# Kernel optimization log

Measured on AMD Instinct MI355X. Metric: run time of the kernel, lower is better.

Reference implementation:

```python
import jax, jax.numpy as jnp
import numpy as np

N_NODES = 50000
N_EDGES = 600000
VOCAB = 50000
D_IN = 256   # embed.output_size
D = 128      # size


def gcn_conv(x, w, b, src, dst, num_nodes):
    # PyG GCNConv: x' = D^{-1/2} (A + I) D^{-1/2} (x @ W^T) + b
    loop = jnp.arange(num_nodes)
    s = jnp.concatenate([src, loop])
    d = jnp.concatenate([dst, loop])
    x = x @ w.T                                           # [N, D]
    deg = jax.ops.segment_sum(jnp.ones_like(s, x.dtype), d, num_segments=num_nodes)
    dinv = jnp.where(deg > 0, jax.lax.rsqrt(deg), 0.0)
    norm = dinv[s] * dinv[d]                              # [E+N]
    msgs = x[s] * norm[:, None]                           # gather + scale
    out = jax.ops.segment_sum(msgs, d, num_segments=num_nodes)  # scatter-add
    return out + b


def setup_inputs() -> dict:
    key = jax.random.key(0)
    ks = jax.random.split(key, 7)
    node_tokens = jax.random.randint(ks[0], (N_NODES,), 0, VOCAB)
    edge_index = jax.random.randint(ks[1], (2, N_EDGES), 0, N_NODES)
    embed_table = jax.random.normal(ks[2], (VOCAB, D_IN), dtype=jnp.float32) * 0.02
    W_node_w = jax.random.normal(ks[3], (D, D_IN), dtype=jnp.float32) * 0.02
    W_node_b = jnp.zeros((D,), dtype=jnp.float32)
    w1 = jax.random.normal(ks[4], (D, D), dtype=jnp.float32) * 0.02
    b1 = jnp.zeros((D,), dtype=jnp.float32)
    w2 = jax.random.normal(ks[5], (D, D), dtype=jnp.float32) * 0.02
    b2 = jnp.zeros((D,), dtype=jnp.float32)
    return {"node_tokens": node_tokens, "edge_index": edge_index,
            "embed_table": embed_table, "W_node_w": W_node_w, "W_node_b": W_node_b,
            "w1": w1, "b1": b1, "w2": w2, "b2": b2}


def reference(node_tokens, edge_index, embed_table, W_node_w, W_node_b, w1, b1, w2, b2):
    src, dst = edge_index[0], edge_index[1]
    e = embed_table[node_tokens]                 # [N, D_IN] embedding lookup
    x = e @ W_node_w.T + W_node_b                # [N, D]
    x = gcn_conv(x, w1, b1, src, dst, N_NODES)
    x = jax.nn.relu(x)
    x = gcn_conv(x, w2, b2, src, dst, N_NODES)
    return x
```

## Files before the change

kernel.cpp:

```cpp
#include <hip/hip_runtime.h>
#include <hip/hip_bf16.h>

#define N_NODES 50000
#define N_EDGES 600000
#define D_IN 256
#define D 128

#define SCAN_CHUNK 1024
#define N_CHUNKS ((N_NODES + SCAN_CHUNK - 1) / SCAN_CHUNK)
#define GEMM_BLOCKS ((N_NODES + 31) / 32)
#define EDGE_BLOCKS ((N_EDGES + 255) / 256)

typedef unsigned short ushort_t;
typedef __attribute__((ext_vector_type(8))) short bf16x8;
typedef __attribute__((ext_vector_type(16))) float f32x16;

__device__ __forceinline__ float bf2f(ushort_t u) {
  union { unsigned int i; float f; } v;
  v.i = ((unsigned int)u) << 16;
  return v.f;
}
__device__ __forceinline__ ushort_t f2bf(float f) {
  union { float f; unsigned int i; } v;
  v.f = f;
  unsigned int x = v.i;
  unsigned int r = (x + 0x7FFFu + ((x >> 16) & 1u)) >> 16;
  return (ushort_t)r;
}


__global__ __launch_bounds__(256) void k_prep_deg(
    const float* __restrict__ wn, const float* __restrict__ w1,
    const float* __restrict__ bn, const float* __restrict__ w2,
    const float* __restrict__ b1, const float* __restrict__ b2,
    const int* __restrict__ dst,
    ushort_t* __restrict__ WcSw, float* __restrict__ bc,
    ushort_t* __restrict__ W2Sw, float* __restrict__ b1f,
    float* __restrict__ b2f, int* __restrict__ deg,
    int* __restrict__ epos) {
  int bid = blockIdx.x;
  if (bid < 128) {
    int j = bid;
    int k = threadIdx.x;
    float acc = 0.f;
    for (int m = 0; m < 128; m++)
      acc += w1[j * 128 + m] * wn[m * 256 + k];
    ushort_t h = f2bf(acc);
    ushort_t l = f2bf(acc - bf2f(h));
    int wv = j >> 5, fm = j & 31;
    int kh = k >> 7, t = (k >> 4) & 7, fq = (k >> 3) & 1, c = k & 7;
    int lane = fq * 32 + fm;
    int base = ((wv * 2 + kh) * 8 + t) * 2 * 512 + lane * 8 + c;
    WcSw[base] = h;
    WcSw[base + 512] = l;
    if (k == 0) {
      float s = 0.f;
      for (int m = 0; m < 128; m++) s += w1[j * 128 + m] * bn[m];
      bc[j] = s;
    }
  } else if (bid < 193) {
    int i = (bid - 128) * 256 + threadIdx.x;
    if (i >= 16640) return;
    if (i < 16384) {
      float v = w2[i];
      ushort_t h = f2bf(v);
      ushort_t l = f2bf(v - bf2f(h));
      int j = i >> 7, k = i & 127;
      int wv = j >> 5, fm = j & 31;
      int t = (k >> 4) & 7, fq = (k >> 3) & 1, c = k & 7;
      int lane = fq * 32 + fm;
      int base = (wv * 8 + t) * 2 * 512 + lane * 8 + c;
      W2Sw[base] = h;
      W2Sw[base + 512] = l;
    } else if (i < 16512) {
      b1f[i - 16384] = b1[i - 16384];
    } else {
      b2f[i - 16512] = b2[i - 16512];
    }
  } else {
    int e = (bid - 193) * 256 + threadIdx.x;
    if (e < N_EDGES) epos[e] = atomicAdd(&deg[dst[e]], 1);
  }
}


__global__ void k_partial(const int* __restrict__ deg, int* __restrict__ partial) {
  __shared__ int lds[256];
  int b = blockIdx.x, t = threadIdx.x;
  int base = b * SCAN_CHUNK + t * 4;
  int s = 0;
#pragma unroll
  for (int i = 0; i < 4; i++) {
    int idx = base + i;
    if (idx < N_NODES) s += deg[idx];
  }
  lds[t] = s;
  __syncthreads();
  for (int off = 128; off > 0; off >>= 1) {
    if (t < off) lds[t] += lds[t + off];
    __syncthreads();
  }
  if (t == 0) partial[b] = lds[0];
}

__global__ void k_scan_final(const int* __restrict__ deg, const int* __restrict__ partial,
                             int* __restrict__ row_start, float* __restrict__ dinv) {
  __shared__ int lds[256];
  __shared__ int plds[64];
  int b = blockIdx.x, t = threadIdx.x;
  if (t < N_CHUNKS) plds[t] = partial[t];
  __syncthreads();
  if (t == 0) {
    int s = 0;
    for (int i = 0; i < b; i++) s += plds[i];
    plds[63] = s;
  }
  int base = b * SCAN_CHUNK + t * 4;
  int v[4];
  int s = 0;
#pragma unroll
  for (int i = 0; i < 4; i++) {
    int idx = base + i;
    v[i] = (idx < N_NODES) ? deg[idx] : 0;
    s += v[i];
  }
  lds[t] = s;
  __syncthreads();
  for (int off = 1; off < 256; off <<= 1) {
    int add = (t >= off) ? lds[t - off] : 0;
    __syncthreads();
    lds[t] += add;
    __syncthreads();
  }
  int excl = lds[t] - s + plds[63];
#pragma unroll
  for (int i = 0; i < 4; i++) {
    int idx = base + i;
    if (idx < N_NODES) {
      row_start[idx] = excl;
      dinv[idx] = rsqrtf((float)(v[i] + 1));
      excl += v[i];
    }
  }
  if (b == 0 && t == 0) row_start[N_NODES] = N_EDGES;
}

__global__ __launch_bounds__(256) void k_gemm_fill(
    const float* __restrict__ Xv, const int* __restrict__ tokens,
    const ushort_t* __restrict__ Wsw,
    const float* __restrict__ bias, const float* __restrict__ dinvp,
    ushort_t* __restrict__ OutT,
    const int* __restrict__ src, const int* __restrict__ dst,
    const int* __restrict__ row_start, const int* __restrict__ epos,
    int* __restrict__ csr) {
  constexpr int KDIM = D_IN;
  constexpr int KH = KDIM / 128;
  constexpr int XS = KDIM + 8;
  __shared__ __align__(16) ushort_t xh_lds[32 * XS];
  __shared__ __align__(16) ushort_t xl_lds[32 * XS];

  int bid = blockIdx.x;
  if (bid >= GEMM_BLOCKS) {
    int e = (bid - GEMM_BLOCKS) * 256 + threadIdx.x;
    if (e < N_EDGES) {
      int d = dst[e];
      csr[row_start[d] + epos[e]] = src[e];
    }
    return;
  }

  int tid = threadIdx.x;
  int lane = tid & 63;
  int wv = tid >> 6;
  int node0 = bid * 32;
  int fm = lane & 31;
  int fq = lane >> 5;

  {
    constexpr int NT = (32 * KDIM / 4) / 256;
    float4 v[NT];
    int rows[NT], cs[NT];
#pragma unroll
    for (int i = 0; i < NT; i++) {
      int seg = tid + 256 * i;
      rows[i] = seg / (KDIM / 4);
      cs[i] = seg % (KDIM / 4);
      int tk = tokens[min(node0 + rows[i], N_NODES - 1)];
      v[i] = *(const float4*)&Xv[(size_t)tk * KDIM + 4 * cs[i]];
    }
#pragma unroll
    for (int i = 0; i < NT; i++) {
      ushort4 h, l;
      h.x = f2bf(v[i].x); l.x = f2bf(v[i].x - bf2f(h.x));
      h.y = f2bf(v[i].y); l.y = f2bf(v[i].y - bf2f(h.y));
      h.z = f2bf(v[i].z); l.z = f2bf(v[i].z - bf2f(h.z));
      h.w = f2bf(v[i].w); l.w = f2bf(v[i].w - bf2f(h.w));
      *(ushort4*)&xh_lds[rows[i] * XS + 4 * cs[i]] = h;
      *(ushort4*)&xl_lds[rows[i] * XS + 4 * cs[i]] = l;
    }
  }
  __syncthreads();

  f32x16 acc;
#pragma unroll
  for (int r = 0; r < 16; r++) acc[r] = 0.f;

#pragma unroll
  for (int kh = 0; kh < KH; kh++) {
    const ushort_t* wb = Wsw + ((size_t)(wv * KH + kh) * 8) * 2 * 512 + lane * 8;
    bf16x8 wbh[8], wbl[8];
#pragma unroll
    for (int t = 0; t < 8; t++) {
      wbh[t] = *(const bf16x8*)(wb + (size_t)t * 1024);
      wbl[t] = *(const bf16x8*)(wb + (size_t)t * 1024 + 512);
    }
#pragma unroll
    for (int t = 0; t < 8; t++) {
      int ko = kh * 128 + t * 16 + fq * 8;
      bf16x8 ah = *(const bf16x8*)&xh_lds[fm * XS + ko];
      bf16x8 al = *(const bf16x8*)&xl_lds[fm * XS + ko];
      acc = __builtin_amdgcn_mfma_f32_32x32x16_bf16(ah, wbh[t], acc, 0, 0, 0);
      acc = __builtin_amdgcn_mfma_f32_32x32x16_bf16(ah, wbl[t], acc, 0, 0, 0);
      acc = __builtin_amdgcn_mfma_f32_32x32x16_bf16(al, wbh[t], acc, 0, 0, 0);
    }
  }
  int j = wv * 32 + fm;
  float bv = bias[j];
#pragma unroll
  for (int r = 0; r < 16; r++) {
    int row = (r & 3) + 8 * (r >> 2) + 4 * fq;
    int node = node0 + row;
    if (node < N_NODES)
      OutT[(size_t)node * D + j] = f2bf((acc[r] + bv) * dinvp[node]);
  }
}

__device__ __forceinline__ void addu4(float acc[8], uint4 u) {
  acc[0] += bf2f((ushort_t)(u.x & 0xFFFFu));
  acc[1] += bf2f((ushort_t)(u.x >> 16));
  acc[2] += bf2f((ushort_t)(u.y & 0xFFFFu));
  acc[3] += bf2f((ushort_t)(u.y >> 16));
  acc[4] += bf2f((ushort_t)(u.z & 0xFFFFu));
  acc[5] += bf2f((ushort_t)(u.z >> 16));
  acc[6] += bf2f((ushort_t)(u.w & 0xFFFFu));
  acc[7] += bf2f((ushort_t)(u.w >> 16));
}

__device__ __forceinline__ void agg_edges4(
    const uint4* __restrict__ tu4, const int* __restrict__ csr,
    int e0, int e1, int lane, int g, int h, float acc[8]) {
  for (int base = e0; base < e1; base += 64) {
    int cnt = min(64, e1 - base);
    int sidx = (lane < cnt) ? csr[base + lane] : 0;
    int i = 0;
    for (; i + 32 <= cnt; i += 32) {
      uint4 u[8];
#pragma unroll
      for (int q = 0; q < 8; q++) {
        int s = __shfl(sidx, i + 4 * q + g);
        u[q] = tu4[(size_t)s * 16 + h];
      }
#pragma unroll
      for (int q = 0; q < 8; q++) addu4(acc, u[q]);
    }
    for (; i + 8 <= cnt; i += 8) {
      uint4 u[2];
#pragma unroll
      for (int q = 0; q < 2; q++) {
        int s = __shfl(sidx, i + 4 * q + g);
        u[q] = tu4[(size_t)s * 16 + h];
      }
      addu4(acc, u[0]);
      addu4(acc, u[1]);
    }
    for (; i + 4 <= cnt; i += 4) {
      int s = __shfl(sidx, i + g);
      uint4 u = tu4[(size_t)s * 16 + h];
      addu4(acc, u);
    }
    if (i < cnt) {
      int r = cnt - i;
      int s = __shfl(sidx, (g < r) ? (i + g) : i);
      uint4 u = tu4[(size_t)s * 16 + h];
      if (g < r) addu4(acc, u);
    }
  }
}

__global__ __launch_bounds__(256) void k_agg_gemm(
    const ushort_t* __restrict__ t1, const int* __restrict__ row_start,
    const int* __restrict__ csr, const float* __restrict__ dinv,
    const float* __restrict__ b1f,
    const ushort_t* __restrict__ Wsw, ushort_t* __restrict__ OutT2) {
  constexpr int XS = 136;
  __shared__ __align__(16) ushort_t xh_lds[32 * XS];
  __shared__ __align__(16) ushort_t xl_lds[32 * XS];

  int tid = threadIdx.x;
  int lane = tid & 63;
  int wv = tid >> 6;
  int node0 = blockIdx.x * 32;
  int fm = lane & 31;
  int fq = lane >> 5;
  int g = lane >> 4;
  int h = lane & 15;

  const uint4* tu4 = (const uint4*)t1;
  float4 bA = *(const float4*)&b1f[h * 8];
  float4 bB = *(const float4*)&b1f[h * 8 + 4];

  for (int rr = 0; rr < 8; rr++) {
    int row = wv * 8 + rr;
    int node = node0 + row;
    float acc[8];
#pragma unroll
    for (int q = 0; q < 8; q++) acc[q] = 0.f;
    if (node < N_NODES)
      agg_edges4(tu4, csr, row_start[node], row_start[node + 1], lane, g, h, acc);
#pragma unroll
    for (int q = 0; q < 8; q++) {
      acc[q] += __shfl_xor(acc[q], 16);
      acc[q] += __shfl_xor(acc[q], 32);
    }
    float v[8];
    if (node < N_NODES) {
      addu4(acc, tu4[(size_t)node * 16 + h]);
      float di = dinv[node];
      v[0] = fmaxf(di * acc[0] + bA.x, 0.f);
      v[1] = fmaxf(di * acc[1] + bA.y, 0.f);
      v[2] = fmaxf(di * acc[2] + bA.z, 0.f);
      v[3] = fmaxf(di * acc[3] + bA.w, 0.f);
      v[4] = fmaxf(di * acc[4] + bB.x, 0.f);
      v[5] = fmaxf(di * acc[5] + bB.y, 0.f);
      v[6] = fmaxf(di * acc[6] + bB.z, 0.f);
      v[7] = fmaxf(di * acc[7] + bB.w, 0.f);
    } else {
#pragma unroll
      for (int q = 0; q < 8; q++) v[q] = 0.f;
    }
    if (g < 2) {
      bf16x8 pack;
#pragma unroll
      for (int q = 0; q < 8; q++) {
        ushort_t hq = f2bf(v[q]);
        pack[q] = (short)((g == 0) ? hq : f2bf(v[q] - bf2f(hq)));
      }
      ushort_t* dstp = (g == 0) ? &xh_lds[row * XS + h * 8]
                                : &xl_lds[row * XS + h * 8];
      *(bf16x8*)dstp = pack;
    }
  }
  __syncthreads();

  f32x16 acc;
#pragma unroll
  for (int r = 0; r < 16; r++) acc[r] = 0.f;
  {
    const ushort_t* wb = Wsw + ((size_t)wv * 8) * 2 * 512 + lane * 8;
    bf16x8 wbh[8], wbl[8];
#pragma unroll
    for (int t = 0; t < 8; t++) {
      wbh[t] = *(const bf16x8*)(wb + (size_t)t * 1024);
      wbl[t] = *(const bf16x8*)(wb + (size_t)t * 1024 + 512);
    }
#pragma unroll
    for (int t = 0; t < 8; t++) {
      int ko = t * 16 + fq * 8;
      bf16x8 ah = *(const bf16x8*)&xh_lds[fm * XS + ko];
      bf16x8 al = *(const bf16x8*)&xl_lds[fm * XS + ko];
      acc = __builtin_amdgcn_mfma_f32_32x32x16_bf16(ah, wbh[t], acc, 0, 0, 0);
      acc = __builtin_amdgcn_mfma_f32_32x32x16_bf16(ah, wbl[t], acc, 0, 0, 0);
      acc = __builtin_amdgcn_mfma_f32_32x32x16_bf16(al, wbh[t], acc, 0, 0, 0);
    }
  }
  int j = wv * 32 + fm;
#pragma unroll
  for (int r = 0; r < 16; r++) {
    int row = (r & 3) + 8 * (r >> 2) + 4 * fq;
    int node = node0 + row;
    if (node < N_NODES)
      OutT2[(size_t)node * D + j] = f2bf(acc[r] * dinv[node]);
  }
}

__global__ __launch_bounds__(256) void k_aggregate_out(
    const ushort_t* __restrict__ t, const int* __restrict__ row_start,
    const int* __restrict__ csr, const float* __restrict__ dinv,
    const float* __restrict__ bias, float* __restrict__ out_f) {
  int wave = threadIdx.x >> 6;
  int lane = threadIdx.x & 63;
  int node = blockIdx.x * 4 + wave;
  if (node >= N_NODES) return;
  int g = lane >> 4;
  int h = lane & 15;
  const uint4* tu4 = (const uint4*)t;
  float acc[8];
#pragma unroll
  for (int q = 0; q < 8; q++) acc[q] = 0.f;
  agg_edges4(tu4, csr, row_start[node], row_start[node + 1], lane, g, h, acc);
#pragma unroll
  for (int q = 0; q < 8; q++) {
    acc[q] += __shfl_xor(acc[q], 16);
    acc[q] += __shfl_xor(acc[q], 32);
  }
  addu4(acc, tu4[(size_t)node * 16 + h]);
  float di = dinv[node];
  float4 bA = *(const float4*)&bias[h * 8];
  float4 bB = *(const float4*)&bias[h * 8 + 4];
  if (g == 0) {
    float4 o;
    o.x = di * acc[0] + bA.x;
    o.y = di * acc[1] + bA.y;
    o.z = di * acc[2] + bA.z;
    o.w = di * acc[3] + bA.w;
    *(float4*)&out_f[(size_t)node * D + h * 8] = o;
  } else if (g == 1) {
    float4 o;
    o.x = di * acc[4] + bB.x;
    o.y = di * acc[5] + bB.y;
    o.z = di * acc[6] + bB.z;
    o.w = di * acc[7] + bB.w;
    *(float4*)&out_f[(size_t)node * D + h * 8 + 4] = o;
  }
}

extern "C" void kernel_launch(void* const* d_in, const int* in_sizes, int n_in,
                              void* d_out, int out_size, void* d_ws, size_t ws_size,
                              hipStream_t stream) {
  const int* tokens = (const int*)d_in[0];
  const int* edge = (const int*)d_in[1];
  const float* embed = (const float*)d_in[2];
  const float* Wn = (const float*)d_in[3];
  const float* bn = (const float*)d_in[4];
  const float* w1 = (const float*)d_in[5];
  const float* b1 = (const float*)d_in[6];
  const float* w2 = (const float*)d_in[7];
  const float* b2 = (const float*)d_in[8];
  float* out = (float*)d_out;

  const int* src = edge;
  const int* dst = edge + N_EDGES;

  char* ws = (char*)d_ws;
  ushort_t* T1 = (ushort_t*)ws;
  ushort_t* T2 = (ushort_t*)(ws + 12800000);
  int* epos = (int*)(ws + 25600000);
  float* dinv = (float*)(ws + 38400000);
  int* row_start = (int*)(ws + 38600064);
  int* deg = (int*)(ws + 38800128);
  int* csr = (int*)(ws + 39200128);
  int* partial = (int*)(ws + 41600192);
  ushort_t* WcSw = (ushort_t*)(ws + 41600512);
  ushort_t* W2Sw = (ushort_t*)(ws + 41731584);
  float* bias_ws = (float*)(ws + 41797120);
  float* bcf = bias_ws;
  float* b1f = bias_ws + 128;
  float* b2f = bias_ws + 256;

  hipMemsetAsync(deg, 0, N_NODES * sizeof(int), stream);
  k_prep_deg<<<193 + EDGE_BLOCKS, 256, 0, stream>>>(
      Wn, w1, bn, w2, b1, b2, dst, WcSw, bcf, W2Sw, b1f, b2f, deg, epos);

  k_partial<<<N_CHUNKS, 256, 0, stream>>>(deg, partial);
  k_scan_final<<<N_CHUNKS, 256, 0, stream>>>(deg, partial, row_start, dinv);

  k_gemm_fill<<<GEMM_BLOCKS + EDGE_BLOCKS, 256, 0, stream>>>(
      embed, tokens, WcSw, bcf, dinv, T1, src, dst, row_start, epos, csr);

  k_agg_gemm<<<GEMM_BLOCKS, 256, 0, stream>>>(
      T1, row_start, csr, dinv, b1f, W2Sw, T2);

  k_aggregate_out<<<(N_NODES + 3) / 4, 256, 0, stream>>>(
      T2, row_start, csr, dinv, b2f, out);
}
```

Baseline: 258.5 us.

## Assign one node per 16-lane group in aggregation instead of one per wave

The edge-aggregation helper now gives each 16-lane quarter-wave its own destination node, so one wave processes four nodes at once. Before, the whole wave split a single node's edges four ways and then combined the partial sums with cross-lane shuffles. The change removes those reduction shuffles and the idle lanes on low-degree nodes (about 12 edges per node), and it loads the row_start bounds once per wave. The cost is more divergence between groups when node degrees differ, and less memory-level parallelism per node. The output kernel now launches four times fewer blocks, and every lane writes both of its float4 outputs.

```diff
diff --git a/kernel.cpp b/kernel.cpp
--- a/kernel.cpp
+++ b/kernel.cpp
@@ -246,43 +246,50 @@
   acc[7] += bf2f((ushort_t)(u.w >> 16));
 }
 
-__device__ __forceinline__ void agg_edges4(
+__device__ __forceinline__ void agg_group(
     const uint4* __restrict__ tu4, const int* __restrict__ csr,
-    int e0, int e1, int lane, int g, int h, float acc[8]) {
-  for (int base = e0; base < e1; base += 64) {
-    int cnt = min(64, e1 - base);
-    int sidx = (lane < cnt) ? csr[base + lane] : 0;
+    int e0, int e1, int lane, int h, float acc[8]) {
+  int gbase = lane & 48;
+  for (int base = e0; base < e1; base += 16) {
+    int cnt = min(16, e1 - base);
+    int sidx = (h < cnt) ? csr[base + h] : 0;
     int i = 0;
-    for (; i + 32 <= cnt; i += 32) {
+    for (; i + 8 <= cnt; i += 8) {
       uint4 u[8];
 #pragma unroll
       for (int q = 0; q < 8; q++) {
-        int s = __shfl(sidx, i + 4 * q + g);
+        int s = __shfl(sidx, gbase + i + q);
         u[q] = tu4[(size_t)s * 16 + h];
       }
 #pragma unroll
       for (int q = 0; q < 8; q++) addu4(acc, u[q]);
     }
-    for (; i + 8 <= cnt; i += 8) {
+    if (i + 4 <= cnt) {
+      uint4 u[4];
+#pragma unroll
+      for (int q = 0; q < 4; q++) {
+        int s = __shfl(sidx, gbase + i + q);
+        u[q] = tu4[(size_t)s * 16 + h];
+      }
+#pragma unroll
+      for (int q = 0; q < 4; q++) addu4(acc, u[q]);
+      i += 4;
+    }
+    if (i + 2 <= cnt) {
       uint4 u[2];
 #pragma unroll
       for (int q = 0; q < 2; q++) {
-        int s = __shfl(sidx, i + 4 * q + g);
+        int s = __shfl(sidx, gbase + i + q);
         u[q] = tu4[(size_t)s * 16 + h];
       }
       addu4(acc, u[0]);
       addu4(acc, u[1]);
-    }
-    for (; i + 4 <= cnt; i += 4) {
-      int s = __shfl(sidx, i + g);
+      i += 2;
+    }
+    if (i < cnt) {
+      int s = __shfl(sidx, gbase + i);
       uint4 u = tu4[(size_t)s * 16 + h];
       addu4(acc, u);
-    }
-    if (i < cnt) {
-      int r = cnt - i;
-      int s = __shfl(sidx, (g < r) ? (i + g) : i);
-      uint4 u = tu4[(size_t)s * 16 + h];
-      if (g < r) addu4(acc, u);
     }
   }
 }
@@ -309,23 +316,27 @@
   float4 bA = *(const float4*)&b1f[h * 8];
   float4 bB = *(const float4*)&b1f[h * 8 + 4];
 
-  for (int rr = 0; rr < 8; rr++) {
-    int row = wv * 8 + rr;
+  int node0w = node0 + wv * 8;
+  int rsv = row_start[min(node0w + min(lane, 8), N_NODES)];
+
+#pragma unroll
+  for (int p = 0; p < 2; p++) {
+    int r = p * 4 + g;
+    int row = wv * 8 + r;
     int node = node0 + row;
+    int e0 = __shfl(rsv, r);
+    int e1 = __shfl(rsv, r + 1);
     float acc[8];
 #pragma unroll
     for (int q = 0; q < 8; q++) acc[q] = 0.f;
-    if (node < N_NODES)
-      agg_edges4(tu4, csr, row_start[node], row_start[node + 1], lane, g, h, acc);
-#pragma unroll
-    for (int q = 0; q < 8; q++) {
-      acc[q] += __shfl_xor(acc[q], 16);
-      acc[q] += __shfl_xor(acc[q], 32);
-    }
-    float v[8];
     if (node < N_NODES) {
+      agg_group(tu4, csr, e0, e1, lane, h, acc);
       addu4(acc, tu4[(size_t)node * 16 + h]);
+    }
+    bf16x8 ph, pl;
+    if (node < N_NODES) {
       float di = dinv[node];
+      float v[8];
       v[0] = fmaxf(di * acc[0] + bA.x, 0.f);
       v[1] = fmaxf(di * acc[1] + bA.y, 0.f);
       v[2] = fmaxf(di * acc[2] + bA.z, 0.f);
@@ -334,21 +345,18 @@
       v[5] = fmaxf(di * acc[5] + bB.y, 0.f);
       v[6] = fmaxf(di * acc[6] + bB.z, 0.f);
       v[7] = fmaxf(di * acc[7] + bB.w, 0.f);
-    } else {
-#pragma unroll
-      for (int q = 0; q < 8; q++) v[q] = 0.f;
-    }
-    if (g < 2) {
-      bf16x8 pack;
 #pragma unroll
       for (int q = 0; q < 8; q++) {
         ushort_t hq = f2bf(v[q]);
-        pack[q] = (short)((g == 0) ? hq : f2bf(v[q] - bf2f(hq)));
+        ph[q] = (short)hq;
+        pl[q] = (short)f2bf(v[q] - bf2f(hq));
       }
-      ushort_t* dstp = (g == 0) ? &xh_lds[row * XS + h * 8]
-                                : &xl_lds[row * XS + h * 8];
-      *(bf16x8*)dstp = pack;
-    }
+    } else {
+#pragma unroll
+      for (int q = 0; q < 8; q++) { ph[q] = 0; pl[q] = 0; }
+    }
+    *(bf16x8*)&xh_lds[row * XS + h * 8] = ph;
+    *(bf16x8*)&xl_lds[row * XS + h * 8] = pl;
   }
   __syncthreads();
 
@@ -387,41 +395,37 @@
     const ushort_t* __restrict__ t, const int* __restrict__ row_start,
     const int* __restrict__ csr, const float* __restrict__ dinv,
     const float* __restrict__ bias, float* __restrict__ out_f) {
-  int wave = threadIdx.x >> 6;
+  int wv = threadIdx.x >> 6;
   int lane = threadIdx.x & 63;
-  int node = blockIdx.x * 4 + wave;
-  if (node >= N_NODES) return;
   int g = lane >> 4;
   int h = lane & 15;
+  int nodew = blockIdx.x * 16 + wv * 4;
+  int rsv = row_start[min(nodew + min(lane, 4), N_NODES)];
+  int node = nodew + g;
+  int e0 = __shfl(rsv, g);
+  int e1 = __shfl(rsv, g + 1);
+  if (node >= N_NODES) return;
+
   const uint4* tu4 = (const uint4*)t;
   float acc[8];
 #pragma unroll
   for (int q = 0; q < 8; q++) acc[q] = 0.f;
-  agg_edges4(tu4, csr, row_start[node], row_start[node + 1], lane, g, h, acc);
-#pragma unroll
-  for (int q = 0; q < 8; q++) {
-    acc[q] += __shfl_xor(acc[q], 16);
-    acc[q] += __shfl_xor(acc[q], 32);
-  }
+  agg_group(tu4, csr, e0, e1, lane, h, acc);
   addu4(acc, tu4[(size_t)node * 16 + h]);
   float di = dinv[node];
   float4 bA = *(const float4*)&bias[h * 8];
   float4 bB = *(const float4*)&bias[h * 8 + 4];
-  if (g == 0) {
-    float4 o;
-    o.x = di * acc[0] + bA.x;
-    o.y = di * acc[1] + bA.y;
-    o.z = di * acc[2] + bA.z;
-    o.w = di * acc[3] + bA.w;
-    *(float4*)&out_f[(size_t)node * D + h * 8] = o;
-  } else if (g == 1) {
-    float4 o;
-    o.x = di * acc[4] + bB.x;
-    o.y = di * acc[5] + bB.y;
-    o.z = di * acc[6] + bB.z;
-    o.w = di * acc[7] + bB.w;
-    *(float4*)&out_f[(size_t)node * D + h * 8 + 4] = o;
-  }
+  float4 o0, o1;
+  o0.x = di * acc[0] + bA.x;
+  o0.y = di * acc[1] + bA.y;
+  o0.z = di * acc[2] + bA.z;
+  o0.w = di * acc[3] + bA.w;
+  o1.x = di * acc[4] + bB.x;
+  o1.y = di * acc[5] + bB.y;
+  o1.z = di * acc[6] + bB.z;
+  o1.w = di * acc[7] + bB.w;
+  *(float4*)&out_f[(size_t)node * D + h * 8] = o0;
+  *(float4*)&out_f[(size_t)node * D + h * 8 + 4] = o1;
 }
 
 extern "C" void kernel_launch(void* const* d_in, const int* in_sizes, int n_in,
@@ -470,6 +474,6 @@
   k_agg_gemm<<<GEMM_BLOCKS, 256, 0, stream>>>(
       T1, row_start, csr, dinv, b1f, W2Sw, T2);
 
-  k_aggregate_out<<<(N_NODES + 3) / 4, 256, 0, stream>>>(
+  k_aggregate_out<<<(N_NODES + 15) / 16, 256, 0, stream>>>(
       T2, row_start, csr, dinv, b2f, out);
 }
```

New measurement: 232.3 us. 10.1% less time.
